# Kernel tuning notes

Hardware: AMD Instinct MI355X
Metric: run time of the kernel (lower is better)

Reference implementation:

```python
import jax, jax.numpy as jnp
import numpy as np

B, N, IN_DIM, D, H, L = 8, 256, 2, 128, 512, 2
EPS = 1e-5


def layer_norm(x, g, b):
    m = jnp.mean(x, axis=-1, keepdims=True)
    v = jnp.var(x, axis=-1, keepdims=True)
    return (x - m) * jax.lax.rsqrt(v + EPS) * g + b


def loo_max_pool(nodes):
    # nodes: (B, N, D) -> leave-one-out max over the set axis -> (B, N, D)
    n = nodes.shape[1]
    neg = jnp.finfo(nodes.dtype).min
    mask = jnp.eye(n, dtype=bool)[None, :, :, None]          # (1, N, N, 1)
    expanded = jnp.broadcast_to(nodes[:, None, :, :],
                                (nodes.shape[0], n, n, nodes.shape[2]))
    return jnp.where(mask, neg, expanded).max(axis=2)        # (B, N, D)


def setup_inputs() -> dict:
    key = jax.random.key(0)
    ks = jax.random.split(key, 16)
    s = 0.02
    inp = {
        "x":   jax.random.normal(ks[0], (B, N, IN_DIM), dtype=jnp.float32),
        # embedding linear + its LayerNorm
        "We":  jax.random.normal(ks[1], (IN_DIM, D)) * s,
        "be":  jnp.zeros((D,), jnp.float32),
        "ge":  jnp.ones((D,), jnp.float32),
        "bge": jnp.zeros((D,), jnp.float32),
        # per-layer pool linear (concat of x and LOO-pooled context: 2D -> D)
        "Wp":  jax.random.normal(ks[2], (L, 2 * D, D)) * s,
        "bp":  jnp.zeros((L, D), jnp.float32),
        "gp":  jnp.ones((L, D), jnp.float32),
        "bgp": jnp.zeros((L, D), jnp.float32),
        # per-layer feed-forward D -> H -> D
        "W1":  jax.random.normal(ks[3], (L, D, H)) * s,
        "b1":  jnp.zeros((L, H), jnp.float32),
        "W2":  jax.random.normal(ks[4], (L, H, D)) * s,
        "b2":  jnp.zeros((L, D), jnp.float32),
        "gf":  jnp.ones((L, D), jnp.float32),
        "bgf": jnp.zeros((L, D), jnp.float32),
    }
    return inp


def reference(x, We, be, ge, bge, Wp, bp, gp, bgp, W1, b1, W2, b2, gf, bgf):
    # embeddings + embedding norm
    h = layer_norm(x @ We + be, ge, bge)                      # (B, N, D)
    for i in range(L):
        # pool layer: LOO max pooling, concat, linear, residual, norm
        pooled = loo_max_pool(h)                              # (B, N, D)
        cat = jnp.concatenate([h, pooled], axis=-1)           # (B, N, 2D)
        h = layer_norm(h + cat @ Wp[i] + bp[i], gp[i], bgp[i])
        # feed-forward, residual, norm
        ff = jax.nn.relu(h @ W1[i] + b1[i]) @ W2[i] + b2[i]
        h = layer_norm(h + ff, gf[i], bgf[i])
    return h
```

## Files before the change

### kernel.cpp

```cpp
#include <hip/hip_runtime.h>
#include <hip/hip_bf16.h>

#define BB 8
#define NN 256
#define DD 128
#define HH 512
#define LL 2
#define EPSV 1e-5f
#define TPB 8
#define BPL (NN/TPB)

typedef unsigned short ushort_t;
typedef __attribute__((ext_vector_type(8))) short bf16x8;
typedef __attribute__((ext_vector_type(4))) float f32x4;

#if defined(__has_builtin)
#if __has_builtin(__builtin_amdgcn_sched_barrier)
#define SCHED_FENCE() __builtin_amdgcn_sched_barrier(0)
#endif
#endif
#ifndef SCHED_FENCE
#define SCHED_FENCE()
#endif

__device__ __forceinline__ ushort_t f2b(float v){
  __hip_bfloat16 h = __float2bfloat16(v);
  return *(ushort_t*)&h;
}

__device__ __forceinline__ void waveRed2(float &a, float &b){
  #pragma unroll
  for (int off=32; off>=1; off>>=1){
    a += __shfl_xor(a, off, 64);
    b += __shfl_xor(b, off, 64);
  }
}

__device__ __forceinline__ void poolMerge(float &m1, float &m2, int &am,
                                          float o1, float o2, int oa){
  if (o1 > m1){ m2 = fmaxf(m1, o2); m1 = o1; am = oa; }
  else        { m2 = fmaxf(m2, o1); }
}

__global__ __launch_bounds__(512, 2) void k_net(
    int layer,
    const float* __restrict__ x, const float* __restrict__ We,
    const float* __restrict__ be, const float* __restrict__ ge,
    const float* __restrict__ bge,
    float* __restrict__ hio,
    float* __restrict__ pm1, float* __restrict__ pm2, int* __restrict__ pma,
    const float* __restrict__ Wp, const float* __restrict__ bp,
    const float* __restrict__ gp, const float* __restrict__ bgp,
    const float* __restrict__ W1, const float* __restrict__ b1,
    const float* __restrict__ W2, const float* __restrict__ b2,
    const float* __restrict__ gf, const float* __restrict__ bgf)
{
  int tid = threadIdx.x;
  int d = tid & 127, fourth = tid >> 7;
  int wv = tid >> 6;
  int lane = tid & 63;
  int m = lane & 15, q = lane >> 4;
  int t0 = blockIdx.x * TPB;
  int b = t0 >> 8;
  int blk = (t0 >> 3) & (BPL-1);

  __shared__ float    hcur[8*128];
  __shared__ ushort_t catb[16*256];
  __shared__ float    sA[16*128];
  __shared__ ushort_t h1b[16*128];
  __shared__ float    h1f[8*128];
  __shared__ ushort_t ub[16*512];
  __shared__ float fm1[128], fm2[128];
  __shared__ int   fam[128];
  __shared__ float sm1[4][128], sm2[4][128];
  __shared__ int   sam[4][128];
  __shared__ float xs[512];
  __shared__ float red9[2][12];
  __shared__ float stats[12];

  if (layer == 0){
    xs[tid] = x[(size_t)b*512 + tid];
    float a = We[d], bw = We[128+d], c = be[d];
    if (fourth == 0){
      float r0=a, r1=bw;        waveRed2(r0,r1);
      float r2=c, r3=a*a;       waveRed2(r2,r3);
      float r4=bw*bw, r5=c*c;   waveRed2(r4,r5);
      float r6=a*bw, r7=a*c;    waveRed2(r6,r7);
      float r8=bw*c, r9=0.f;    waveRed2(r8,r9);
      int w = (tid >> 6) & 1;
      if (lane == 0){
        red9[w][0]=r0; red9[w][1]=r1; red9[w][2]=r2; red9[w][3]=r3;
        red9[w][4]=r4; red9[w][5]=r5; red9[w][6]=r6; red9[w][7]=r7;
        red9[w][8]=r8;
      }
    }
    __syncthreads();
    if (tid < 9) stats[tid] = (red9[0][tid] + red9[1][tid]) * (1.f/128);
    __syncthreads();
    float mA=stats[0], mB=stats[1], mC=stats[2];
    float SAA=stats[3], SBB=stats[4], SCC=stats[5];
    float SAB=stats[6], SAC=stats[7], SBC=stats[8];
    float gev = ge[d], bgev = bge[d];
    float m1=-3.4e38f, m2=-3.4e38f; int am=0;
    for (int i=0;i<64;++i){
      int n = fourth*64 + i;
      float x0 = xs[2*n], x1 = xs[2*n+1];
      float v    = fmaf(x0, a,  fmaf(x1, bw, c));
      float mean = fmaf(x0, mA, fmaf(x1, mB, mC));
      float ev2  = x0*x0*SAA + x1*x1*SBB + SCC
                 + 2.f*(x0*x1*SAB + x0*SAC + x1*SBC);
      float var = ev2 - mean*mean;
      float hv = (v-mean)*rsqrtf(var+EPSV)*gev + bgev;
      poolMerge(m1,m2,am, hv, -3.4e38f, n);
    }
    sm1[fourth][d]=m1; sm2[fourth][d]=m2; sam[fourth][d]=am;
    #pragma unroll
    for (int rep=0; rep<2; ++rep){
      int t = fourth*2 + rep;
      int n = (t0 & 255) + t;
      float x0 = xs[2*n], x1 = xs[2*n+1];
      float v    = fmaf(x0, a,  fmaf(x1, bw, c));
      float mean = fmaf(x0, mA, fmaf(x1, mB, mC));
      float ev2  = x0*x0*SAA + x1*x1*SBB + SCC
                 + 2.f*(x0*x1*SAB + x0*SAC + x1*SBC);
      float var = ev2 - mean*mean;
      hcur[t*128 + d] = (v-mean)*rsqrtf(var+EPSV)*gev + bgev;
    }
    __syncthreads();
  } else {
    {
      size_t base = ((size_t)b*BPL + fourth*8)*128 + d;
      float m1 = pm1[base], m2 = pm2[base]; int am = pma[base];
      #pragma unroll
      for (int i=1;i<8;++i)
        poolMerge(m1,m2,am, pm1[base+(size_t)i*128], pm2[base+(size_t)i*128],
                  pma[base+(size_t)i*128]);
      sm1[fourth][d]=m1; sm2[fourth][d]=m2; sam[fourth][d]=am;
    }
    #pragma unroll
    for (int rep=0; rep<2; ++rep){
      int t = fourth*2 + rep;
      hcur[t*128 + d] = hio[(size_t)(t0+t)*DD + d];
    }
    __syncthreads();
  }

  if (fourth==0){
    float m1=sm1[0][d], m2=sm2[0][d]; int am=sam[0][d];
    #pragma unroll
    for (int p=1;p<4;++p) poolMerge(m1,m2,am, sm1[p][d], sm2[p][d], sam[p][d]);
    fm1[d]=m1; fm2[d]=m2; fam[d]=am;
  }
  __syncthreads();

  #pragma unroll
  for (int rep=0; rep<4; ++rep){
    int e = rep*512 + tid;
    int t = e >> 8, c = e & 255;
    int n = (t0 & 255) + t;
    float v;
    if (c < DD) v = hcur[t*128 + c];
    else { int cc = c - DD; v = (n==fam[cc]) ? fm2[cc] : fm1[cc]; }
    catb[t*256 + c] = f2b(v);
  }
  __syncthreads();

  int n0a = wv*16;

  {
    float wA[8][8];
    #pragma unroll
    for (int ks=0; ks<8; ++ks)
      #pragma unroll
      for (int j=0; j<8; ++j)
        wA[ks][j] = Wp[(size_t)(ks*32 + q*8 + j)*128 + n0a + m];
    SCHED_FENCE();
    f32x4 acc = {0.f,0.f,0.f,0.f};
    const ushort_t* ap = catb + m*256 + q*8;
    #pragma unroll
    for (int ks=0; ks<8; ++ks){
      bf16x8 wf;
      #pragma unroll
      for (int j=0;j<8;++j) wf[j] = (short)f2b(wA[ks][j]);
      bf16x8 af = *(const bf16x8*)(ap + ks*32);
      acc = __builtin_amdgcn_mfma_f32_16x16x32_bf16(af, wf, acc, 0,0,0);
    }
    #pragma unroll
    for (int r=0;r<4;++r) sA[(q*4+r)*128 + n0a + m] = acc[r];
  }
  __syncthreads();

  {
    int t = wv, g = lane;
    float2 v2 = *(const float2*)&sA[t*128 + 2*g];
    float v0 = v2.x + bp[2*g]   + hcur[t*128 + 2*g];
    float v1 = v2.y + bp[2*g+1] + hcur[t*128 + 2*g + 1];
    float s = v0+v1, qq = v0*v0 + v1*v1;
    waveRed2(s,qq);
    float mean = s*(1.f/128), var = qq*(1.f/128) - mean*mean;
    float rs = rsqrtf(var + EPSV);
    float o0 = (v0-mean)*rs*gp[2*g]   + bgp[2*g];
    float o1 = (v1-mean)*rs*gp[2*g+1] + bgp[2*g+1];
    unsigned pk = (unsigned)f2b(o0) | ((unsigned)f2b(o1) << 16);
    *(unsigned*)&h1b[t*128 + 2*g] = pk;
    *(float2*)&h1f[t*128 + 2*g] = make_float2(o0, o1);
  }
  __syncthreads();

  {
    const ushort_t* ap = h1b + m*128 + q*8;
    bf16x8 af[4];
    #pragma unroll
    for (int ks=0; ks<4; ++ks) af[ks] = *(const bf16x8*)(ap + ks*32);
    #pragma unroll
    for (int half=0; half<2; ++half){
      float wB[8][8];
      #pragma unroll
      for (int i=0;i<2;++i){
        int n0 = (half*2+i)*128 + wv*16;
        #pragma unroll
        for (int ks=0; ks<4; ++ks)
          #pragma unroll
          for (int j=0;j<8;++j)
            wB[i*4+ks][j] = W1[(size_t)(ks*32 + q*8 + j)*512 + n0 + m];
      }
      SCHED_FENCE();
      #pragma unroll
      for (int i=0;i<2;++i){
        int n0 = (half*2+i)*128 + wv*16;
        f32x4 acc = {0.f,0.f,0.f,0.f};
        #pragma unroll
        for (int ks=0; ks<4; ++ks){
          bf16x8 wf;
          #pragma unroll
          for (int j=0;j<8;++j) wf[j] = (short)f2b(wB[i*4+ks][j]);
          acc = __builtin_amdgcn_mfma_f32_16x16x32_bf16(af[ks], wf, acc, 0,0,0);
        }
        float bb = b1[n0+m];
        #pragma unroll
        for (int r=0;r<4;++r)
          ub[(q*4+r)*512 + n0 + m] = f2b(fmaxf(acc[r] + bb, 0.f));
      }
    }
  }
  __syncthreads();

  {
    f32x4 acc = {0.f,0.f,0.f,0.f};
    const ushort_t* ap = ub + m*512 + q*8;
    #pragma unroll
    for (int half=0; half<2; ++half){
      float wC[8][8];
      #pragma unroll
      for (int ks=0; ks<8; ++ks)
        #pragma unroll
        for (int j=0;j<8;++j)
          wC[ks][j] = W2[(size_t)((half*8+ks)*32 + q*8 + j)*128 + n0a + m];
      SCHED_FENCE();
      #pragma unroll
      for (int ks=0; ks<8; ++ks){
        bf16x8 wf;
        #pragma unroll
        for (int j=0;j<8;++j) wf[j] = (short)f2b(wC[ks][j]);
        bf16x8 af = *(const bf16x8*)(ap + (half*8+ks)*32);
        acc = __builtin_amdgcn_mfma_f32_16x16x32_bf16(af, wf, acc, 0,0,0);
      }
    }
    #pragma unroll
    for (int r=0;r<4;++r) sA[(q*4+r)*128 + n0a + m] = acc[r];
  }
  __syncthreads();

  {
    int t = wv, g = lane;
    float2 v2 = *(const float2*)&sA[t*128 + 2*g];
    float v0 = v2.x + b2[2*g]   + h1f[t*128 + 2*g];
    float v1 = v2.y + b2[2*g+1] + h1f[t*128 + 2*g + 1];
    float s = v0+v1, qq = v0*v0 + v1*v1;
    waveRed2(s,qq);
    float mean = s*(1.f/128), var = qq*(1.f/128) - mean*mean;
    float rs = rsqrtf(var + EPSV);
    float o0 = (v0-mean)*rs*gf[2*g]   + bgf[2*g];
    float o1 = (v1-mean)*rs*gf[2*g+1] + bgf[2*g+1];
    *(float2*)&hio[(size_t)(t0+t)*DD + 2*g] = make_float2(o0, o1);
    *(float2*)&hcur[t*128 + 2*g] = make_float2(o0, o1);
  }
  if (layer == 0){
    __syncthreads();
    if (tid < 128){
      int n0 = t0 & 255;
      float m1 = hcur[tid], m2 = -3.4e38f; int am = n0;
      #pragma unroll
      for (int p=1;p<TPB;++p)
        poolMerge(m1,m2,am, hcur[p*128+tid], -3.4e38f, n0+p);
      size_t idx = ((size_t)b*BPL + blk)*128 + tid;
      pm1[idx]=m1; pm2[idx]=m2; pma[idx]=am;
    }
  }
}

extern "C" void kernel_launch(void* const* d_in, const int* in_sizes, int n_in,
                              void* d_out, int out_size, void* d_ws, size_t ws_size,
                              hipStream_t stream)
{
  const float* x   = (const float*)d_in[0];
  const float* We  = (const float*)d_in[1];
  const float* be  = (const float*)d_in[2];
  const float* ge  = (const float*)d_in[3];
  const float* bge = (const float*)d_in[4];
  const float* Wp  = (const float*)d_in[5];
  const float* bp  = (const float*)d_in[6];
  const float* gp  = (const float*)d_in[7];
  const float* bgp = (const float*)d_in[8];
  const float* W1  = (const float*)d_in[9];
  const float* b1  = (const float*)d_in[10];
  const float* W2  = (const float*)d_in[11];
  const float* b2  = (const float*)d_in[12];
  const float* gf  = (const float*)d_in[13];
  const float* bgf = (const float*)d_in[14];

  float* hio = (float*)d_out;
  char* ws = (char*)d_ws;
  const size_t NP = (size_t)BB*BPL*128;
  float* p1 = (float*)ws;            ws += NP*4;
  float* p2 = (float*)ws;            ws += NP*4;
  int*   pa = (int*)ws;              ws += NP*4;

  const int grid = (BB*NN)/TPB;

  k_net<<<grid, 512, 0, stream>>>(0, x, We, be, ge, bge, hio, p1, p2, pa,
      Wp,                    bp,      gp,      bgp,
      W1,                    b1,      W2,      b2,
      gf,                    bgf);

  k_net<<<grid, 512, 0, stream>>>(1, x, We, be, ge, bge, hio, p1, p2, pa,
      Wp + (size_t)2*DD*DD,  bp + DD, gp + DD, bgp + DD,
      W1 + (size_t)DD*HH,    b1 + HH, W2 + (size_t)HH*DD, b2 + DD,
      gf + DD,               bgf + DD);
}
```

Before: 115.4 us.

## Prepack weights to bf16 MFMA fragment layout and swizzle LDS activation tiles

A new prep kernel converts Wp, W1 and W2 to bf16 once per call and stores them in the per-lane MFMA fragment order. Each wave of the main kernel can then load its weight fragment with one 16-byte vector load, instead of 8 strided scalar fp32 loads plus in-register conversion. The LDS activation buffers (catb, h1b, ub) also get an XOR swizzle to avoid bank conflicts on the 16-byte fragment reads. The cost is an extra kernel launch and workspace traffic for the converted weights.

New measurement: 108.4 us. 1.06x faster.

```diff
diff --git a/kernel.cpp b/kernel.cpp
--- a/kernel.cpp
+++ b/kernel.cpp
@@ -14,14 +14,11 @@
 typedef __attribute__((ext_vector_type(8))) short bf16x8;
 typedef __attribute__((ext_vector_type(4))) float f32x4;
 
-#if defined(__has_builtin)
-#if __has_builtin(__builtin_amdgcn_sched_barrier)
-#define SCHED_FENCE() __builtin_amdgcn_sched_barrier(0)
-#endif
-#endif
-#ifndef SCHED_FENCE
-#define SCHED_FENCE()
-#endif
+#define WPSZ (256*128)
+#define W1SZ (128*512)
+#define W2SZ (512*128)
+#define LAYSZ (WPSZ+W1SZ+W2SZ)
+#define TOTW (2*LAYSZ)
 
 __device__ __forceinline__ ushort_t f2b(float v){
   __hip_bfloat16 h = __float2bfloat16(v);
@@ -40,6 +37,31 @@
                                           float o1, float o2, int oa){
   if (o1 > m1){ m2 = fmaxf(m1, o2); m1 = o1; am = oa; }
   else        { m2 = fmaxf(m2, o1); }
+}
+
+__global__ __launch_bounds__(512) void k_prep(
+    const float* __restrict__ Wp, const float* __restrict__ W1,
+    const float* __restrict__ W2, ushort_t* __restrict__ wcvt)
+{
+  int e8 = blockIdx.x*512 + threadIdx.x;
+  if (e8 >= TOTW/8) return;
+  int e = e8*8;
+  int l2 = (e >= LAYSZ) ? 1 : 0;
+  int el = e - l2*LAYSZ;
+  const float* src; int N, KSlog, off;
+  if (el < WPSZ)           { src = Wp + (size_t)l2*WPSZ; N = 128; KSlog = 3; off = el; }
+  else if (el < WPSZ+W1SZ) { src = W1 + (size_t)l2*W1SZ; N = 512; KSlog = 2; off = el - WPSZ; }
+  else                     { src = W2 + (size_t)l2*W2SZ; N = 128; KSlog = 4; off = el - (WPSZ+W1SZ); }
+  int rec  = off >> 9;
+  int ln   = (off >> 3) & 63;
+  int n0t  = rec >> KSlog;
+  int ks   = rec & ((1<<KSlog)-1);
+  int row0 = ks*32 + ((ln>>4)<<3);
+  int col  = (n0t<<4) + (ln&15);
+  bf16x8 v;
+  #pragma unroll
+  for (int j=0;j<8;++j) v[j] = (short)f2b(src[(size_t)(row0+j)*N + col]);
+  *(bf16x8*)(wcvt + e) = v;
 }
 
 __global__ __launch_bounds__(512, 2) void k_net(
@@ -49,10 +71,11 @@
     const float* __restrict__ bge,
     float* __restrict__ hio,
     float* __restrict__ pm1, float* __restrict__ pm2, int* __restrict__ pma,
-    const float* __restrict__ Wp, const float* __restrict__ bp,
+    const ushort_t* __restrict__ wL,
+    const float* __restrict__ bp,
     const float* __restrict__ gp, const float* __restrict__ bgp,
-    const float* __restrict__ W1, const float* __restrict__ b1,
-    const float* __restrict__ W2, const float* __restrict__ b2,
+    const float* __restrict__ b1,
+    const float* __restrict__ b2,
     const float* __restrict__ gf, const float* __restrict__ bgf)
 {
   int tid = threadIdx.x;
@@ -63,6 +86,11 @@
   int t0 = blockIdx.x * TPB;
   int b = t0 >> 8;
   int blk = (t0 >> 3) & (BPL-1);
+  int n0a = wv*16;
+
+  const ushort_t* wAb = wL;
+  const ushort_t* wBb = wL + WPSZ;
+  const ushort_t* wCb = wL + WPSZ + W1SZ;
 
   __shared__ float    hcur[8*128];
   __shared__ ushort_t catb[16*256];
@@ -156,33 +184,24 @@
   #pragma unroll
   for (int rep=0; rep<4; ++rep){
     int e = rep*512 + tid;
-    int t = e >> 8, c = e & 255;
+    int t = e >> 8, cc = e & 255;
     int n = (t0 & 255) + t;
     float v;
-    if (c < DD) v = hcur[t*128 + c];
-    else { int cc = c - DD; v = (n==fam[cc]) ? fm2[cc] : fm1[cc]; }
-    catb[t*256 + c] = f2b(v);
-  }
-  __syncthreads();
-
-  int n0a = wv*16;
-
-  {
-    float wA[8][8];
-    #pragma unroll
-    for (int ks=0; ks<8; ++ks)
-      #pragma unroll
-      for (int j=0; j<8; ++j)
-        wA[ks][j] = Wp[(size_t)(ks*32 + q*8 + j)*128 + n0a + m];
-    SCHED_FENCE();
+    if (cc < DD) v = hcur[t*128 + cc];
+    else { int c2 = cc - DD; v = (n==fam[c2]) ? fm2[c2] : fm1[c2]; }
+    *(ushort_t*)((char*)catb + ((e*2) ^ ((t&7)<<4))) = f2b(v);
+  }
+  __syncthreads();
+
+  {
     f32x4 acc = {0.f,0.f,0.f,0.f};
-    const ushort_t* ap = catb + m*256 + q*8;
+    const char* apb = (const char*)catb;
+    int abase = (m*256 + q*8)*2;
+    int sw = (m&7)<<4;
     #pragma unroll
     for (int ks=0; ks<8; ++ks){
-      bf16x8 wf;
-      #pragma unroll
-      for (int j=0;j<8;++j) wf[j] = (short)f2b(wA[ks][j]);
-      bf16x8 af = *(const bf16x8*)(ap + ks*32);
+      bf16x8 wf = *(const bf16x8*)(wAb + ((size_t)(wv*8+ks)*64 + lane)*8);
+      bf16x8 af = *(const bf16x8*)(apb + ((abase + ks*64) ^ sw));
       acc = __builtin_amdgcn_mfma_f32_16x16x32_bf16(af, wf, acc, 0,0,0);
     }
     #pragma unroll
@@ -202,44 +221,38 @@
     float o0 = (v0-mean)*rs*gp[2*g]   + bgp[2*g];
     float o1 = (v1-mean)*rs*gp[2*g+1] + bgp[2*g+1];
     unsigned pk = (unsigned)f2b(o0) | ((unsigned)f2b(o1) << 16);
-    *(unsigned*)&h1b[t*128 + 2*g] = pk;
+    *(unsigned*)((char*)h1b + (((t*128 + 2*g)*2) ^ ((t&7)<<4))) = pk;
     *(float2*)&h1f[t*128 + 2*g] = make_float2(o0, o1);
   }
   __syncthreads();
 
   {
-    const ushort_t* ap = h1b + m*128 + q*8;
+    const char* apb = (const char*)h1b;
+    int abase = (m*128 + q*8)*2;
+    int sw = (m&7)<<4;
     bf16x8 af[4];
     #pragma unroll
-    for (int ks=0; ks<4; ++ks) af[ks] = *(const bf16x8*)(ap + ks*32);
+    for (int ks=0; ks<4; ++ks)
+      af[ks] = *(const bf16x8*)(apb + ((abase + ks*64) ^ sw));
     #pragma unroll
     for (int half=0; half<2; ++half){
-      float wB[8][8];
       #pragma unroll
       for (int i=0;i<2;++i){
         int n0 = (half*2+i)*128 + wv*16;
-        #pragma unroll
-        for (int ks=0; ks<4; ++ks)
-          #pragma unroll
-          for (int j=0;j<8;++j)
-            wB[i*4+ks][j] = W1[(size_t)(ks*32 + q*8 + j)*512 + n0 + m];
-      }
-      SCHED_FENCE();
-      #pragma unroll
-      for (int i=0;i<2;++i){
-        int n0 = (half*2+i)*128 + wv*16;
+        int n0t = (half*2+i)*8 + wv;
         f32x4 acc = {0.f,0.f,0.f,0.f};
         #pragma unroll
         for (int ks=0; ks<4; ++ks){
-          bf16x8 wf;
-          #pragma unroll
-          for (int j=0;j<8;++j) wf[j] = (short)f2b(wB[i*4+ks][j]);
+          bf16x8 wf = *(const bf16x8*)(wBb + ((size_t)(n0t*4+ks)*64 + lane)*8);
           acc = __builtin_amdgcn_mfma_f32_16x16x32_bf16(af[ks], wf, acc, 0,0,0);
         }
         float bb = b1[n0+m];
         #pragma unroll
-        for (int r=0;r<4;++r)
-          ub[(q*4+r)*512 + n0 + m] = f2b(fmaxf(acc[r] + bb, 0.f));
+        for (int r=0;r<4;++r){
+          int row = q*4+r;
+          *(ushort_t*)((char*)ub + (((row*512 + n0 + m)*2) ^ ((row&7)<<4)))
+              = f2b(fmaxf(acc[r] + bb, 0.f));
+        }
       }
     }
   }
@@ -247,24 +260,14 @@
 
   {
     f32x4 acc = {0.f,0.f,0.f,0.f};
-    const ushort_t* ap = ub + m*512 + q*8;
-    #pragma unroll
-    for (int half=0; half<2; ++half){
-      float wC[8][8];
-      #pragma unroll
-      for (int ks=0; ks<8; ++ks)
-        #pragma unroll
-        for (int j=0;j<8;++j)
-          wC[ks][j] = W2[(size_t)((half*8+ks)*32 + q*8 + j)*128 + n0a + m];
-      SCHED_FENCE();
-      #pragma unroll
-      for (int ks=0; ks<8; ++ks){
-        bf16x8 wf;
-        #pragma unroll
-        for (int j=0;j<8;++j) wf[j] = (short)f2b(wC[ks][j]);
-        bf16x8 af = *(const bf16x8*)(ap + (half*8+ks)*32);
-        acc = __builtin_amdgcn_mfma_f32_16x16x32_bf16(af, wf, acc, 0,0,0);
-      }
+    const char* apb = (const char*)ub;
+    int abase = (m*512 + q*8)*2;
+    int sw = (m&7)<<4;
+    #pragma unroll
+    for (int kk=0; kk<16; ++kk){
+      bf16x8 wf = *(const bf16x8*)(wCb + ((size_t)(wv*16+kk)*64 + lane)*8);
+      bf16x8 af = *(const bf16x8*)(apb + ((abase + kk*64) ^ sw));
+      acc = __builtin_amdgcn_mfma_f32_16x16x32_bf16(af, wf, acc, 0,0,0);
     }
     #pragma unroll
     for (int r=0;r<4;++r) sA[(q*4+r)*128 + n0a + m] = acc[r];
@@ -325,16 +328,21 @@
   float* p1 = (float*)ws;            ws += NP*4;
   float* p2 = (float*)ws;            ws += NP*4;
   int*   pa = (int*)ws;              ws += NP*4;
+  ushort_t* wcvt = (ushort_t*)ws;
 
   const int grid = (BB*NN)/TPB;
 
+  k_prep<<<80, 512, 0, stream>>>(Wp, W1, W2, wcvt);
+
   k_net<<<grid, 512, 0, stream>>>(0, x, We, be, ge, bge, hio, p1, p2, pa,
-      Wp,                    bp,      gp,      bgp,
-      W1,                    b1,      W2,      b2,
-      gf,                    bgf);
+      wcvt,
+      bp,      gp,      bgp,
+      b1,      b2,
+      gf,      bgf);
 
   k_net<<<grid, 512, 0, stream>>>(1, x, We, be, ge, bge, hio, p1, p2, pa,
-      Wp + (size_t)2*DD*DD,  bp + DD, gp + DD, bgp + DD,
-      W1 + (size_t)DD*HH,    b1 + HH, W2 + (size_t)HH*DD, b2 + DD,
-      gf + DD,               bgf + DD);
-}
+      wcvt + LAYSZ,
+      bp + DD, gp + DD, bgp + DD,
+      b1 + HH, b2 + DD,
+      gf + DD, bgf + DD);
+}
```
